# Optimization experiments

Measured on AMD Instinct MI355X. Metric: run time of the kernel, lower is better.

Reference implementation:

```python
import jax, jax.numpy as jnp
import numpy as np

WEIGHT = 1.0

# OpenCV RGB->Lab constants (D65 white point, 8-bit scaling)
_XN = 0.950456
_ZN = 1.088754
_T0 = 0.008856  # (6/29)^3 threshold


def _rgb_to_lab_cv8(rgb):
    """Differentiable analogue of cv2.cvtColor(uint8, COLOR_RGB2LAB)/255.
    rgb: [B,3,H,W] in [0,1]. Returns [B,3,H,W] with L/100, (a+128)/255, (b+128)/255.
    (Skips the non-differentiable uint8 quantization of the original.)"""
    r, g, b = rgb[:, 0], rgb[:, 1], rgb[:, 2]
    x = (0.412453 * r + 0.357580 * g + 0.180423 * b) / _XN
    y = 0.212671 * r + 0.715160 * g + 0.072169 * b
    z = (0.019334 * r + 0.119193 * g + 0.950227 * b) / _ZN

    def f(t):
        return jnp.where(t > _T0, jnp.cbrt(jnp.maximum(t, _T0)), 7.787 * t + 16.0 / 116.0)

    fx, fy, fz = f(x), f(y), f(z)
    L = jnp.where(y > _T0, 116.0 * fy - 16.0, 903.3 * y)  # 0..100
    a = 500.0 * (fx - fy)
    bb = 200.0 * (fy - fz)
    # cv2 8-bit scaling: L*255/100, a+128, b+128; original divides by 255 afterwards
    return jnp.stack([L / 100.0, (a + 128.0) / 255.0, (bb + 128.0) / 255.0], axis=1)


def setup_inputs() -> dict:
    key = jax.random.key(0)
    k1, k2 = jax.random.split(key)
    shape = (16, 3, 512, 512)
    pred = jax.random.uniform(k1, shape, dtype=jnp.float32)
    target = jax.random.uniform(k2, shape, dtype=jnp.float32)
    return {"pred": pred, "target": target}


def reference(pred, target):
    pred_lab = _rgb_to_lab_cv8(pred)
    target_lab = _rgb_to_lab_cv8(target)
    loss = jnp.mean((pred_lab - target_lab) ** 2)
    return WEIGHT * loss
```

## Files before the change

### kernel.cpp

```cpp
#include <hip/hip_runtime.h>

#define HW       262144
#define HWV      65536
#define CH       HW
#define BSTRIDE  (3*HW)
#define NELEM_INV (1.0f / 12582912.0f)

#define GRID1    4096
#define BLOCK1   256

typedef float f4 __attribute__((ext_vector_type(4)));
typedef float f2 __attribute__((ext_vector_type(2)));

__device__ __forceinline__ f4 vload(const float* p) {
    return *reinterpret_cast<const f4*>(p);
}

__device__ __forceinline__ f2 f_lab2(f2 t) {
    const float T0 = 0.008856f;
    f2 lg;
    lg.x = __builtin_amdgcn_logf(t.x);
    lg.y = __builtin_amdgcn_logf(t.y);
    f2 e = lg * 0.33333333333333f;
    f2 cb;
    cb.x = __builtin_amdgcn_exp2f(e.x);
    cb.y = __builtin_amdgcn_exp2f(e.y);
    f2 lin = __builtin_elementwise_fma(f2{7.787f, 7.787f}, t,
                                       f2{16.0f / 116.0f, 16.0f / 116.0f});
    f2 r;
    r.x = (t.x > T0) ? cb.x : lin.x;
    r.y = (t.y > T0) ? cb.y : lin.y;
    return r;
}

__device__ __forceinline__ float pix_loss2(f2 r, f2 g, f2 b) {
    f2 x = __builtin_elementwise_fma(f2{0.433953f, 0.433953f}, r,
           __builtin_elementwise_fma(f2{0.376219f, 0.376219f}, g,
                                     g * 0.0f + b * 0.189828f));
    f2 y = __builtin_elementwise_fma(f2{0.212671f, 0.212671f}, r,
           __builtin_elementwise_fma(f2{0.715160f, 0.715160f}, g, b * 0.072169f));
    f2 z = __builtin_elementwise_fma(f2{0.017758f, 0.017758f}, r,
           __builtin_elementwise_fma(f2{0.109477f, 0.109477f}, g, b * 0.872766f));
    f2 fx = f_lab2(x);
    f2 fy = f_lab2(y);
    f2 fz = f_lab2(z);
    float u = fx.x - fx.y;
    float v = fy.x - fy.y;
    float w = fz.x - fz.y;
    float dL = 1.16f * v;
    float da = (u - v) * (500.0f / 255.0f);
    float db = (v - w) * (200.0f / 255.0f);
    return fmaf(dL, dL, fmaf(da, da, db * db));
}

__device__ __forceinline__ float quad_loss(const f4& pr, const f4& pg, const f4& pb,
                                           const f4& tr, const f4& tg, const f4& tb) {
    float a;
    a  = pix_loss2(f2{pr.x, tr.x}, f2{pg.x, tg.x}, f2{pb.x, tb.x});
    a += pix_loss2(f2{pr.y, tr.y}, f2{pg.y, tg.y}, f2{pb.y, tb.y});
    a += pix_loss2(f2{pr.z, tr.z}, f2{pg.z, tg.z}, f2{pb.z, tb.z});
    a += pix_loss2(f2{pr.w, tr.w}, f2{pg.w, tg.w}, f2{pb.w, tb.w});
    return a;
}

__global__ __launch_bounds__(BLOCK1, 8) void cc_partial(
        const float* __restrict__ pred,
        const float* __restrict__ tgt,
        float* __restrict__ part) {
    const int vbase = blockIdx.x << 8;
    const int batch = vbase >> 16;
    const size_t ebase = (size_t)batch * BSTRIDE + (size_t)((vbase & (HWV - 1)) << 2);

    const float* pp = pred + ebase + (threadIdx.x << 2);
    const float* tp = tgt  + ebase + (threadIdx.x << 2);

    const f4 pr = vload(pp);
    const f4 pg = vload(pp + CH);
    const f4 pb = vload(pp + 2 * CH);
    const f4 tr = vload(tp);
    const f4 tg = vload(tp + CH);
    const f4 tb = vload(tp + 2 * CH);

    float acc = quad_loss(pr, pg, pb, tr, tg, tb);

    #pragma unroll
    for (int off = 32; off > 0; off >>= 1)
        acc += __shfl_down(acc, off);

    __shared__ float smem[BLOCK1 / 64];
    const int lane = threadIdx.x & 63;
    const int wid  = threadIdx.x >> 6;
    if (lane == 0) smem[wid] = acc;
    __syncthreads();
    if (threadIdx.x == 0) {
        float s = 0.0f;
        #pragma unroll
        for (int w = 0; w < BLOCK1 / 64; ++w) s += smem[w];
        part[blockIdx.x] = s;
    }
}

__global__ __launch_bounds__(256) void cc_final(
        const float* __restrict__ part,
        float* __restrict__ out) {
    const float* p = part + (threadIdx.x << 4);
    f4 a0 = vload(p);
    f4 a1 = vload(p + 4);
    f4 a2 = vload(p + 8);
    f4 a3 = vload(p + 12);
    float acc = (a0.x + a0.y + a0.z + a0.w) + (a1.x + a1.y + a1.z + a1.w)
              + (a2.x + a2.y + a2.z + a2.w) + (a3.x + a3.y + a3.z + a3.w);

    #pragma unroll
    for (int off = 32; off > 0; off >>= 1)
        acc += __shfl_down(acc, off);

    __shared__ float smem[4];
    const int lane = threadIdx.x & 63;
    const int wid  = threadIdx.x >> 6;
    if (lane == 0) smem[wid] = acc;
    __syncthreads();
    if (threadIdx.x == 0) {
        float s = smem[0] + smem[1] + smem[2] + smem[3];
        out[0] = s * NELEM_INV;
    }
}

extern "C" void kernel_launch(void* const* d_in, const int* in_sizes, int n_in,
                              void* d_out, int out_size, void* d_ws, size_t ws_size,
                              hipStream_t stream) {
    const float* pred = (const float*)d_in[0];
    const float* tgt  = (const float*)d_in[1];
    float* out  = (float*)d_out;
    float* part = (float*)d_ws;

    cc_partial<<<GRID1, BLOCK1, 0, stream>>>(pred, tgt, part);
    cc_final<<<1, 256, 0, stream>>>(part, out);
}
```

Baseline: 23.60 us.

## Fuse final reduction via fixed-point atomic accumulation and last-block ticket

Replaces the second reduction kernel with a deterministic 64-bit fixed-point atomicAdd of each block's partial sum, plus a ticket counter so the last block writes the mean. A hipMemsetAsync zeroes the accumulator and ticket before launch, so one kernel launch becomes a memset plus a kernel. It also drops a redundant g*0 term in the x computation. This costs 8192 global atomics, and the memset adds its own small launch overhead.

New measurement: 75.13 us. 3.18x slower.

```diff
diff --git a/kernel.cpp b/kernel.cpp
--- a/kernel.cpp
+++ b/kernel.cpp
@@ -8,6 +8,9 @@
 
 #define GRID1    4096
 #define BLOCK1   256
+
+#define FIXSCALE   68719476736.0
+#define FIXSCALE_I (1.0 / 68719476736.0)
 
 typedef float f4 __attribute__((ext_vector_type(4)));
 typedef float f2 __attribute__((ext_vector_type(2)));
@@ -35,8 +38,7 @@
 
 __device__ __forceinline__ float pix_loss2(f2 r, f2 g, f2 b) {
     f2 x = __builtin_elementwise_fma(f2{0.433953f, 0.433953f}, r,
-           __builtin_elementwise_fma(f2{0.376219f, 0.376219f}, g,
-                                     g * 0.0f + b * 0.189828f));
+           __builtin_elementwise_fma(f2{0.376219f, 0.376219f}, g, b * 0.189828f));
     f2 y = __builtin_elementwise_fma(f2{0.212671f, 0.212671f}, r,
            __builtin_elementwise_fma(f2{0.715160f, 0.715160f}, g, b * 0.072169f));
     f2 z = __builtin_elementwise_fma(f2{0.017758f, 0.017758f}, r,
@@ -63,10 +65,12 @@
     return a;
 }
 
-__global__ __launch_bounds__(BLOCK1, 8) void cc_partial(
+__global__ __launch_bounds__(BLOCK1, 8) void cc_fused(
         const float* __restrict__ pred,
         const float* __restrict__ tgt,
-        float* __restrict__ part) {
+        unsigned long long* __restrict__ acc,
+        unsigned* __restrict__ ticket,
+        float* __restrict__ out) {
     const int vbase = blockIdx.x << 8;
     const int batch = vbase >> 16;
     const size_t ebase = (size_t)batch * BSTRIDE + (size_t)((vbase & (HWV - 1)) << 2);
@@ -81,48 +85,32 @@
     const f4 tg = vload(tp + CH);
     const f4 tb = vload(tp + 2 * CH);
 
-    float acc = quad_loss(pr, pg, pb, tr, tg, tb);
+    float a = quad_loss(pr, pg, pb, tr, tg, tb);
 
     #pragma unroll
     for (int off = 32; off > 0; off >>= 1)
-        acc += __shfl_down(acc, off);
+        a += __shfl_down(a, off);
 
     __shared__ float smem[BLOCK1 / 64];
     const int lane = threadIdx.x & 63;
     const int wid  = threadIdx.x >> 6;
-    if (lane == 0) smem[wid] = acc;
+    if (lane == 0) smem[wid] = a;
     __syncthreads();
+
     if (threadIdx.x == 0) {
         float s = 0.0f;
         #pragma unroll
         for (int w = 0; w < BLOCK1 / 64; ++w) s += smem[w];
-        part[blockIdx.x] = s;
-    }
-}
 
-__global__ __launch_bounds__(256) void cc_final(
-        const float* __restrict__ part,
-        float* __restrict__ out) {
-    const float* p = part + (threadIdx.x << 4);
-    f4 a0 = vload(p);
-    f4 a1 = vload(p + 4);
-    f4 a2 = vload(p + 8);
-    f4 a3 = vload(p + 12);
-    float acc = (a0.x + a0.y + a0.z + a0.w) + (a1.x + a1.y + a1.z + a1.w)
-              + (a2.x + a2.y + a2.z + a2.w) + (a3.x + a3.y + a3.z + a3.w);
+        unsigned long long q = (unsigned long long)(long long)llrint((double)s * FIXSCALE);
+        unsigned long long old = atomicAdd(acc, q);
+        asm volatile("s_waitcnt vmcnt(0)" :: "v"(old) : "memory");
 
-    #pragma unroll
-    for (int off = 32; off > 0; off >>= 1)
-        acc += __shfl_down(acc, off);
-
-    __shared__ float smem[4];
-    const int lane = threadIdx.x & 63;
-    const int wid  = threadIdx.x >> 6;
-    if (lane == 0) smem[wid] = acc;
-    __syncthreads();
-    if (threadIdx.x == 0) {
-        float s = smem[0] + smem[1] + smem[2] + smem[3];
-        out[0] = s * NELEM_INV;
+        unsigned told = atomicAdd(ticket, 1u);
+        if (told == GRID1 - 1) {
+            unsigned long long tot = atomicAdd(acc, 0ULL);
+            out[0] = (float)((double)tot * FIXSCALE_I * (double)NELEM_INV);
+        }
     }
 }
 
@@ -131,9 +119,11 @@
                               hipStream_t stream) {
     const float* pred = (const float*)d_in[0];
     const float* tgt  = (const float*)d_in[1];
-    float* out  = (float*)d_out;
-    float* part = (float*)d_ws;
+    float* out = (float*)d_out;
 
-    cc_partial<<<GRID1, BLOCK1, 0, stream>>>(pred, tgt, part);
-    cc_final<<<1, 256, 0, stream>>>(part, out);
+    unsigned long long* acc = (unsigned long long*)d_ws;
+    unsigned* ticket = (unsigned*)((char*)d_ws + 128);
+
+    (void)hipMemsetAsync(d_ws, 0, 136, stream);
+    cc_fused<<<GRID1, BLOCK1, 0, stream>>>(pred, tgt, acc, ticket, out);
 }
```
